# Performance work log

Measured on AMD Instinct MI355X. Metric: run time of the kernel, lower is better.

Reference implementation:

```python
import jax, jax.numpy as jnp
import numpy as np

B, C_IN, H, W = 8, 64, 64, 64
C_OUT = 128
K, STRIDE, PAD = 3, 1, 1
GRID_MIN, GRID_MAX, NUM_GRIDS = -2.0, 2.0, 8
FEAT = C_IN * K * K  # 576


def setup_inputs() -> dict:
    key = jax.random.key(0)
    k1, k2, k3 = jax.random.split(key, 3)
    x = jax.random.normal(k1, (B, C_IN, H, W), dtype=jnp.float32)
    grid = jnp.linspace(GRID_MIN, GRID_MAX, NUM_GRIDS, dtype=jnp.float32)
    spline_weight = jax.random.normal(k2, (FEAT * NUM_GRIDS, C_OUT), dtype=jnp.float32) * 0.1
    # nn.Linear default init ~ U(-1/sqrt(in), 1/sqrt(in)); stored as (in, out) for x @ W
    bound = 1.0 / np.sqrt(FEAT)
    kw, kb = jax.random.split(k3)
    base_w = jax.random.uniform(kw, (FEAT, C_OUT), dtype=jnp.float32, minval=-bound, maxval=bound)
    base_b = jax.random.uniform(kb, (C_OUT,), dtype=jnp.float32, minval=-bound, maxval=bound)
    return {"x": x, "grid": grid, "spline_weight": spline_weight,
            "base_w": base_w, "base_b": base_b}


def reference(x, grid, spline_weight, base_w, base_b):
    b, c, h, w = x.shape
    # F.unfold equivalent: patches in (channel, kh, kw) channel-major order.
    patches = jax.lax.conv_general_dilated_patches(
        x, filter_shape=(K, K), window_strides=(STRIDE, STRIDE),
        padding=((PAD, PAD), (PAD, PAD)))  # [B, C*K*K, H', W']
    oh, ow = patches.shape[2], patches.shape[3]
    # -> [B*L, FEAT] rows, matching unfold().transpose(1,2).reshape(...)
    p = patches.reshape(b, FEAT, oh * ow).transpose(0, 2, 1).reshape(-1, FEAT)
    # RBF basis expansion: exp(-((x - g) / h)^2), h = grid spacing
    denom = (GRID_MAX - GRID_MIN) / (NUM_GRIDS - 1)
    basis = jnp.exp(-(((p[:, :, None] - grid) / denom) ** 2))  # [N, FEAT, G]
    ret = basis.reshape(p.shape[0], FEAT * NUM_GRIDS) @ spline_weight  # [N, C_OUT]
    ret = ret + jax.nn.silu(p) @ base_w + base_b
    # [B, L, C_OUT] -> [B, C_OUT, H', W']
    out = ret.reshape(b, oh * ow, C_OUT).transpose(0, 2, 1).reshape(b, C_OUT, oh, ow)
    return out
```

## Files before the change

### kernel.cpp

```cpp
#include <hip/hip_runtime.h>

#define C_IN   64
#define HW_DIM 64
#define C_OUT  128
#define NG     8
#define KSPL   4608
#define BM     64
#define NSPL_STEPS 72
#define NSTEPS 81
#define NPAD   66
#define NEXP   (8 * C_IN * NPAD * NPAD)

#define WT_BYTES 1327104
#define XE_OFF   WT_BYTES
#define XE_BYTES (NEXP * NG * 2)
#define SE_OFF   (XE_OFF + XE_BYTES)

typedef __attribute__((ext_vector_type(8))) __bf16 bf16x8;
typedef __attribute__((ext_vector_type(4))) float  f32x4;

__global__ __launch_bounds__(256)
void prep_wt(const float* __restrict__ sw, const float* __restrict__ bw,
             __bf16* __restrict__ wt3)
{
  const int step = blockIdx.x;
  const int t    = threadIdx.x;
  const int wc   = t >> 6;
  const int lane = t & 63;
  const int l15  = lane & 15;
  const int g4   = lane >> 4;
#pragma unroll
  for (int n = 0; n < 2; ++n)
#pragma unroll
    for (int ks = 0; ks < 2; ++ks) {
      const int co = wc * 32 + n * 16 + l15;
      bf16x8 v;
#pragma unroll
      for (int e = 0; e < 8; ++e) {
        const int k = step * 64 + ks * 32 + g4 * 8 + e;
        float f;
        if (k < KSPL) f = sw[(size_t)k * C_OUT + co];
        else          f = bw[(size_t)(k - KSPL) * C_OUT + co];
        v[e] = (__bf16)f;
      }
      *(bf16x8*)(wt3 + (size_t)step * 8192 + wc * 2048 + (n * 2 + ks) * 512
                 + lane * 8) = v;
    }
}

__global__ __launch_bounds__(256)
void expand(const float* __restrict__ x, const float* __restrict__ grid,
            __bf16* __restrict__ xe, __bf16* __restrict__ se)
{
  const int idx = blockIdx.x * 256 + threadIdx.x;
  if (idx >= NEXP) return;
  const int xp = idx % NPAD;
  const int r  = idx / NPAD;
  const int yp = r % NPAD;
  const int bc = r / NPAD;

  float p = 0.f;
  if (xp >= 1 && xp <= HW_DIM && yp >= 1 && yp <= HW_DIM)
    p = x[(size_t)bc * (HW_DIM * HW_DIM) + (yp - 1) * HW_DIM + (xp - 1)];

  bf16x8 v;
#pragma unroll
  for (int g = 0; g < NG; ++g) {
    const float z = 1.75f * (p - grid[g]);
    v[g] = (__bf16)__expf(-z * z);
  }
  *(bf16x8*)(xe + (size_t)idx * NG) = v;
  const float e = __expf(-p);
  se[idx] = (__bf16)(p * __builtin_amdgcn_rcpf(1.f + e));
}

static __device__ __forceinline__ void gload16(const __bf16* g, __bf16* l) {
  __builtin_amdgcn_global_load_lds(
      (const __attribute__((address_space(1))) void*)g,
      (__attribute__((address_space(3))) void*)l, 16, 0, 0);
}

#define WAITBAR6() do {                                      \
    asm volatile("s_waitcnt vmcnt(6)" ::: "memory");         \
    __builtin_amdgcn_s_barrier();                            \
    __builtin_amdgcn_sched_barrier(0);                       \
  } while (0)

__global__ __launch_bounds__(256, 2)
void kan_gemm(const __bf16* __restrict__ xe, const __bf16* __restrict__ se,
              const __bf16* __restrict__ wt3, const float* __restrict__ base_b,
              float* __restrict__ out)
{
  __shared__ __align__(16) __bf16 As[3][BM][64];
  __shared__ int tbl[576];

  const int t    = threadIdx.x;
  const int lane = t & 63;
  const int wid  = t >> 6;
  const int l15  = lane & 15;
  const int g4   = lane >> 4;

  const int bid = blockIdx.x;
  const int swz = (bid & 7) * 64 + (bid >> 3);
  const int b   = swz >> 6;
  const int y0  = swz & 63;

  for (int f = t; f < 576; f += 256) {
    const int c  = f / 9;
    const int j  = f - 9 * c;
    const int kh = j / 3;
    const int kw = j - 3 * kh;
    tbl[f] = c * 4356 + kh * 66 + kw;
  }

  const int ROW = b * 278784 + y0 * 66;

  const int qsrc  = (lane & 7) ^ ((lane >> 3) & 7);
  const int pbase = (wid << 3) + (lane >> 3);

  f32x4 acc[2][4];
#pragma unroll
  for (int n = 0; n < 2; ++n)
#pragma unroll
    for (int m = 0; m < 4; ++m)
      acc[n][m] = f32x4{0.f, 0.f, 0.f, 0.f};

  auto stageA = [&](int buf, int step) {
    const int off = ROW + tbl[step * 8 + qsrc] + pbase;
    __bf16* dst = &As[buf][0][0] + t * 8;
    gload16(xe + (size_t)off * 8,        dst);
    gload16(xe + (size_t)(off + 32) * 8, dst + 2048);
  };

  auto loadB = [&](bf16x8 (&wf)[2][2], int step) {
    const __bf16* wb = wt3 + (size_t)step * 8192 + wid * 2048 + lane * 8;
#pragma unroll
    for (int n = 0; n < 2; ++n)
#pragma unroll
      for (int ks = 0; ks < 2; ++ks)
        wf[n][ks] = *(const bf16x8*)(wb + (n * 2 + ks) * 512);
  };

  auto compute = [&](int buf, bf16x8 (&wf)[2][2]) {
    bf16x8 xf[4][2];
#pragma unroll
    for (int ks = 0; ks < 2; ++ks)
#pragma unroll
      for (int m = 0; m < 4; ++m) {
        const int pr = m * 16 + l15;
        xf[m][ks] = *(const bf16x8*)(&As[buf][pr][(((ks * 4 + g4) ^ (pr & 7)) * 8)]);
      }
#pragma unroll
    for (int ks = 0; ks < 2; ++ks)
#pragma unroll
      for (int n = 0; n < 2; ++n)
#pragma unroll
        for (int m = 0; m < 4; ++m)
          acc[n][m] = __builtin_amdgcn_mfma_f32_16x16x32_bf16(
              wf[n][ks], xf[m][ks], acc[n][m], 0, 0, 0);
  };

  __syncthreads();

  bf16x8 wA[2][2], wB[2][2], wC[2][2];
  stageA(0, 0); loadB(wA, 0);
  stageA(1, 1); loadB(wB, 1);
  WAITBAR6();

  for (int s = 0; s < 69; s += 3) {
    stageA(2, s + 2); loadB(wC, s + 2);
    compute(0, wA);
    WAITBAR6();
    stageA(0, s + 3); loadB(wA, s + 3);
    compute(1, wB);
    WAITBAR6();
    stageA(1, s + 4); loadB(wB, s + 4);
    compute(2, wC);
    WAITBAR6();
  }
  stageA(2, 71); loadB(wC, 71);
  compute(0, wA);
  WAITBAR6();
  compute(1, wB);
  asm volatile("s_waitcnt vmcnt(0)" ::: "memory");
  __builtin_amdgcn_s_barrier();
  __builtin_amdgcn_sched_barrier(0);
  compute(2, wC);

  const int ROWs = ROW + (t & 63);
  auto stageBase = [&](int buf, int bs) {
    const int px = t & 63;
#pragma unroll
    for (int h = 0; h < 2; ++h) {
      const int q = (t >> 6) + h * 4;
      bf16x8 v;
#pragma unroll
      for (int jj = 0; jj < 8; ++jj) {
        const int f = (bs - NSPL_STEPS) * 64 + q * 8 + jj;
        v[jj] = se[(size_t)(ROWs + tbl[f])];
      }
      *(bf16x8*)(&As[buf][px][(q ^ (px & 7)) * 8]) = v;
    }
  };

  stageBase(0, NSPL_STEPS);
  __syncthreads();
  for (int bs = NSPL_STEPS; bs < NSTEPS; ++bs) {
    const int cb = (bs - NSPL_STEPS) & 1;
    if (bs + 1 < NSTEPS) stageBase(cb ^ 1, bs + 1);
    loadB(wA, bs);
    compute(cb, wA);
    __syncthreads();
  }

#pragma unroll
  for (int n = 0; n < 2; ++n) {
    const int co = wid * 32 + n * 16 + g4 * 4;
#pragma unroll
    for (int m = 0; m < 4; ++m) {
      const int pl = m * 16 + l15;
      float* o = out + (size_t)(b * C_OUT + co) * 4096 + y0 * 64 + pl;
#pragma unroll
      for (int i = 0; i < 4; ++i)
        o[(size_t)i * 4096] = acc[n][m][i] + base_b[co + i];
    }
  }
}

extern "C" void kernel_launch(void* const* d_in, const int* in_sizes, int n_in,
                              void* d_out, int out_size, void* d_ws, size_t ws_size,
                              hipStream_t stream) {
  const float* x    = (const float*)d_in[0];
  const float* grid = (const float*)d_in[1];
  const float* sw   = (const float*)d_in[2];
  const float* bw   = (const float*)d_in[3];
  const float* bb   = (const float*)d_in[4];
  float* out = (float*)d_out;

  __bf16* wt3 = (__bf16*)d_ws;
  __bf16* xe  = (__bf16*)((char*)d_ws + XE_OFF);
  __bf16* se  = (__bf16*)((char*)d_ws + SE_OFF);

  prep_wt<<<NSTEPS, 256, 0, stream>>>(sw, bw, wt3);
  expand<<<(NEXP + 255) / 256, 256, 0, stream>>>(x, grid, xe, se);
  kan_gemm<<<512, 256, 0, stream>>>(xe, se, wt3, bb, out);
}
```

Before: 78.85 us.

## Relayout expanded activations channel-grouped so GEMM staging is contiguous

The expanded RBF and SiLU tensors move from channel-major padded images to a layout of [b][y][channel group][x][8 channels][8 grids], and the weight K-ordering is permuted to match. Each GEMM step then loads contiguous 16-byte rows without the offset table, and base staging becomes vector loads instead of eight scalar gathers. The expand kernel is split into two LDS-transposing kernels that produce the new layouts. In exchange there is an extra launch and more index arithmetic in expand and prep, and the weight permutation has to match the new K order exactly.

```diff
diff --git a/kernel.cpp b/kernel.cpp
--- a/kernel.cpp
+++ b/kernel.cpp
@@ -4,16 +4,23 @@
 #define HW_DIM 64
 #define C_OUT  128
 #define NG     8
-#define KSPL   4608
 #define BM     64
 #define NSPL_STEPS 72
 #define NSTEPS 81
+#define NBASE  9
 #define NPAD   66
-#define NEXP   (8 * C_IN * NPAD * NPAD)
+
+#define XE_XP   64
+#define XE_GRP  4224
+#define XE_YP   33792
+#define XE_B    2230272
+#define SE_XP   64
+#define SE_YP   4224
+#define SE_B    278784
 
 #define WT_BYTES 1327104
 #define XE_OFF   WT_BYTES
-#define XE_BYTES (NEXP * NG * 2)
+#define XE_BYTES (XE_B * 8 * 2)
 #define SE_OFF   (XE_OFF + XE_BYTES)
 
 typedef __attribute__((ext_vector_type(8))) __bf16 bf16x8;
@@ -23,7 +30,7 @@
 void prep_wt(const float* __restrict__ sw, const float* __restrict__ bw,
              __bf16* __restrict__ wt3)
 {
-  const int step = blockIdx.x;
+  const int bid  = blockIdx.x;
   const int t    = threadIdx.x;
   const int wc   = t >> 6;
   const int lane = t & 63;
@@ -34,44 +41,86 @@
 #pragma unroll
     for (int ks = 0; ks < 2; ++ks) {
       const int co = wc * 32 + n * 16 + l15;
+      const int q  = ks * 4 + g4;
       bf16x8 v;
-#pragma unroll
-      for (int e = 0; e < 8; ++e) {
-        const int k = step * 64 + ks * 32 + g4 * 8 + e;
-        float f;
-        if (k < KSPL) f = sw[(size_t)k * C_OUT + co];
-        else          f = bw[(size_t)(k - KSPL) * C_OUT + co];
-        v[e] = (__bf16)f;
+      if (bid < NSPL_STEPS) {
+        const int grp = bid / 9, j = bid - 9 * grp;
+        const int c   = grp * 8 + q;
+#pragma unroll
+        for (int e = 0; e < 8; ++e)
+          v[e] = (__bf16)sw[(size_t)((c * 9 + j) * 8 + e) * C_OUT + co];
+      } else {
+        const int j = bid - NSPL_STEPS;
+#pragma unroll
+        for (int e = 0; e < 8; ++e)
+          v[e] = (__bf16)bw[(size_t)((q * 8 + e) * 9 + j) * C_OUT + co];
       }
-      *(bf16x8*)(wt3 + (size_t)step * 8192 + wc * 2048 + (n * 2 + ks) * 512
+      *(bf16x8*)(wt3 + (size_t)bid * 8192 + wc * 2048 + (n * 2 + ks) * 512
                  + lane * 8) = v;
     }
 }
 
 __global__ __launch_bounds__(256)
-void expand(const float* __restrict__ x, const float* __restrict__ grid,
-            __bf16* __restrict__ xe, __bf16* __restrict__ se)
-{
-  const int idx = blockIdx.x * 256 + threadIdx.x;
-  if (idx >= NEXP) return;
-  const int xp = idx % NPAD;
-  const int r  = idx / NPAD;
-  const int yp = r % NPAD;
-  const int bc = r / NPAD;
-
-  float p = 0.f;
-  if (xp >= 1 && xp <= HW_DIM && yp >= 1 && yp <= HW_DIM)
-    p = x[(size_t)bc * (HW_DIM * HW_DIM) + (yp - 1) * HW_DIM + (xp - 1)];
-
-  bf16x8 v;
-#pragma unroll
-  for (int g = 0; g < NG; ++g) {
-    const float z = 1.75f * (p - grid[g]);
-    v[g] = (__bf16)__expf(-z * z);
-  }
-  *(bf16x8*)(xe + (size_t)idx * NG) = v;
-  const float e = __expf(-p);
-  se[idx] = (__bf16)(p * __builtin_amdgcn_rcpf(1.f + e));
+void expand_xe(const float* __restrict__ x, const float* __restrict__ grid,
+               __bf16* __restrict__ xe)
+{
+  __shared__ __align__(16) __bf16 buf[528 * 8];
+  const int bid = blockIdx.x;
+  const int b   = bid / 528;
+  const int r   = bid - b * 528;
+  const int yp  = r >> 3;
+  const int grp = r & 7;
+  const int t   = threadIdx.x;
+
+  float gv[NG];
+#pragma unroll
+  for (int g = 0; g < NG; ++g) gv[g] = grid[g];
+
+  for (int i = t; i < 528; i += 256) {
+    const int xp = i >> 3;
+    const int cg = i & 7;
+    const int c  = grp * 8 + cg;
+    float p = 0.f;
+    if (xp >= 1 && xp <= HW_DIM && yp >= 1 && yp <= HW_DIM)
+      p = x[(size_t)(b * C_IN + c) * (HW_DIM * HW_DIM)
+            + (yp - 1) * HW_DIM + (xp - 1)];
+    bf16x8 v;
+#pragma unroll
+    for (int g = 0; g < NG; ++g) {
+      const float z = 1.75f * (p - gv[g]);
+      v[g] = (__bf16)__expf(-z * z);
+    }
+    *(bf16x8*)(buf + i * 8) = v;
+  }
+  __syncthreads();
+  __bf16* dst = xe + (size_t)b * XE_B + yp * XE_YP + grp * XE_GRP;
+  for (int i = t; i < 528; i += 256)
+    *(bf16x8*)(dst + i * 8) = *(const bf16x8*)(buf + i * 8);
+}
+
+__global__ __launch_bounds__(256)
+void expand_se(const float* __restrict__ x, __bf16* __restrict__ se)
+{
+  __shared__ __align__(16) __bf16 buf[4224];
+  const int bid = blockIdx.x;
+  const int b   = bid / 66;
+  const int yp  = bid - b * 66;
+  const int t   = threadIdx.x;
+
+  for (int i = t; i < 4224; i += 256) {
+    const int xp = i >> 6;
+    const int c  = i & 63;
+    float p = 0.f;
+    if (xp >= 1 && xp <= HW_DIM && yp >= 1 && yp <= HW_DIM)
+      p = x[(size_t)(b * C_IN + c) * (HW_DIM * HW_DIM)
+            + (yp - 1) * HW_DIM + (xp - 1)];
+    const float e = __expf(-p);
+    buf[i] = (__bf16)(p * __builtin_amdgcn_rcpf(1.f + e));
+  }
+  __syncthreads();
+  __bf16* dst = se + (size_t)b * SE_B + yp * SE_YP;
+  for (int i = t; i < 528; i += 256)
+    *(bf16x8*)(dst + i * 8) = *(const bf16x8*)(buf + i * 8);
 }
 
 static __device__ __forceinline__ void gload16(const __bf16* g, __bf16* l) {
@@ -92,7 +141,6 @@
               float* __restrict__ out)
 {
   __shared__ __align__(16) __bf16 As[3][BM][64];
-  __shared__ int tbl[576];
 
   const int t    = threadIdx.x;
   const int lane = t & 63;
@@ -105,18 +153,8 @@
   const int b   = swz >> 6;
   const int y0  = swz & 63;
 
-  for (int f = t; f < 576; f += 256) {
-    const int c  = f / 9;
-    const int j  = f - 9 * c;
-    const int kh = j / 3;
-    const int kw = j - 3 * kh;
-    tbl[f] = c * 4356 + kh * 66 + kw;
-  }
-
-  const int ROW = b * 278784 + y0 * 66;
-
-  const int qsrc  = (lane & 7) ^ ((lane >> 3) & 7);
-  const int pbase = (wid << 3) + (lane >> 3);
+  const int px0 = t >> 3;
+  const int qs  = (t & 7) ^ (px0 & 7);
 
   f32x4 acc[2][4];
 #pragma unroll
@@ -125,11 +163,16 @@
     for (int m = 0; m < 4; ++m)
       acc[n][m] = f32x4{0.f, 0.f, 0.f, 0.f};
 
-  auto stageA = [&](int buf, int step) {
-    const int off = ROW + tbl[step * 8 + qsrc] + pbase;
+  const __bf16* xeb = xe + (size_t)b * XE_B + y0 * XE_YP;
+
+  auto stageA = [&](int buf, int s) {
+    const int grp = s / 9, j = s - 9 * grp;
+    const int kh = j / 3, kw = j - 3 * (j / 3);
+    const __bf16* src = xeb + kh * XE_YP + grp * XE_GRP + kw * XE_XP
+                      + px0 * 64 + qs * 8;
     __bf16* dst = &As[buf][0][0] + t * 8;
-    gload16(xe + (size_t)off * 8,        dst);
-    gload16(xe + (size_t)(off + 32) * 8, dst + 2048);
+    gload16(src,        dst);
+    gload16(src + 2048, dst + 2048);
   };
 
   auto loadB = [&](bf16x8 (&wf)[2][2], int step) {
@@ -160,14 +203,12 @@
               wf[n][ks], xf[m][ks], acc[n][m], 0, 0, 0);
   };
 
-  __syncthreads();
-
   bf16x8 wA[2][2], wB[2][2], wC[2][2];
   stageA(0, 0); loadB(wA, 0);
   stageA(1, 1); loadB(wB, 1);
   WAITBAR6();
 
-  for (int s = 0; s < 69; s += 3) {
+  for (int s = 0; s < NSPL_STEPS - 3; s += 3) {
     stageA(2, s + 2); loadB(wC, s + 2);
     compute(0, wA);
     WAITBAR6();
@@ -187,28 +228,25 @@
   __builtin_amdgcn_sched_barrier(0);
   compute(2, wC);
 
-  const int ROWs = ROW + (t & 63);
-  auto stageBase = [&](int buf, int bs) {
+  const __bf16* seb = se + (size_t)b * SE_B + y0 * SE_YP;
+  auto stageBase = [&](int buf, int j) {
+    const int kh = j / 3, kw = j - 3 * (j / 3);
     const int px = t & 63;
+    const __bf16* src = seb + kh * SE_YP + (px + kw) * SE_XP;
 #pragma unroll
     for (int h = 0; h < 2; ++h) {
       const int q = (t >> 6) + h * 4;
-      bf16x8 v;
-#pragma unroll
-      for (int jj = 0; jj < 8; ++jj) {
-        const int f = (bs - NSPL_STEPS) * 64 + q * 8 + jj;
-        v[jj] = se[(size_t)(ROWs + tbl[f])];
-      }
-      *(bf16x8*)(&As[buf][px][(q ^ (px & 7)) * 8]) = v;
-    }
-  };
-
-  stageBase(0, NSPL_STEPS);
+      const bf16x8 v = *(const bf16x8*)(src + q * 8);
+      *(bf16x8*)(&As[buf][px][((q ^ (px & 7)) * 8)]) = v;
+    }
+  };
+
+  stageBase(0, 0);
   __syncthreads();
-  for (int bs = NSPL_STEPS; bs < NSTEPS; ++bs) {
-    const int cb = (bs - NSPL_STEPS) & 1;
-    if (bs + 1 < NSTEPS) stageBase(cb ^ 1, bs + 1);
-    loadB(wA, bs);
+  for (int bs = 0; bs < NBASE; ++bs) {
+    const int cb = bs & 1;
+    if (bs + 1 < NBASE) stageBase(cb ^ 1, bs + 1);
+    loadB(wA, NSPL_STEPS + bs);
     compute(cb, wA);
     __syncthreads();
   }
@@ -242,6 +280,7 @@
   __bf16* se  = (__bf16*)((char*)d_ws + SE_OFF);
 
   prep_wt<<<NSTEPS, 256, 0, stream>>>(sw, bw, wt3);
-  expand<<<(NEXP + 255) / 256, 256, 0, stream>>>(x, grid, xe, se);
+  expand_xe<<<4224, 256, 0, stream>>>(x, grid, xe);
+  expand_se<<<528, 256, 0, stream>>>(x, se);
   kan_gemm<<<512, 256, 0, stream>>>(xe, se, wt3, bb, out);
 }
```

Result: slower. 82.40 us (+4.5%).
